# Kernel tuning notes

Measured on AMD Instinct MI355X. Metric: run time of the kernel, lower is better.

## Reference

```python
import jax, jax.numpy as jnp
import numpy as np

N_SRC = 16384
N_NBR = 16384
E = 524288
D = 128
ALPHA = 0.2  # leaky_relu slope


def setup_inputs() -> dict:
    key = jax.random.key(0)
    ks = jax.random.split(key, 16)
    s = lambda k, shape, fan: jax.random.normal(k, shape, jnp.float32) / np.sqrt(fan)
    x_cur = jax.random.normal(ks[0], (N_SRC, D), jnp.float32)
    x_nbr = jax.random.normal(ks[1], (N_NBR, D), jnp.float32)
    W1c = s(ks[2], (D, D), D); b1c = jnp.zeros((D,), jnp.float32)
    W2c = s(ks[3], (D, D), D); b2c = jnp.zeros((D,), jnp.float32)
    W1n = s(ks[4], (D, D), D); b1n = jnp.zeros((D,), jnp.float32)
    W2n = s(ks[5], (D, D), D); b2n = jnp.zeros((D,), jnp.float32)
    Wa = s(ks[6], (2 * D, 1), 2 * D); ba = jnp.zeros((1,), jnp.float32)
    src = jax.random.randint(ks[7], (E,), 0, N_SRC, jnp.int32)
    dst = jax.random.randint(ks[8], (E,), 0, N_NBR, jnp.int32)
    edges = jnp.stack([src, dst], axis=1)  # [E, 2]
    return dict(x_cur=x_cur, x_nbr=x_nbr, W1c=W1c, b1c=b1c, W2c=W2c, b2c=b2c,
                W1n=W1n, b1n=b1n, W2n=W2n, b2n=b2n, Wa=Wa, ba=ba, edges=edges)


def reference(x_cur, x_nbr, W1c, b1c, W2c, b2c, W1n, b1n, W2n, b2n, Wa, ba, edges):
    src, dst = edges[:, 0], edges[:, 1]
    # hidden MLPs (keras Dense with default activation=None -> linear stack)
    cur = (x_cur @ W1c + b1c) @ W2c + b2c          # [N_src, D]
    nbr = (x_nbr @ W1n + b1n) @ W2n + b2n          # [N_nbr, D]
    # per-edge gather + concat + attention MLP
    pair = jnp.concatenate([cur[src], nbr[dst]], axis=1)   # [E, 2D]
    scores = jax.nn.leaky_relu((pair @ Wa + ba)[:, 0], ALPHA)  # [E]
    # segment softmax over source node
    exp_s = jnp.exp(scores)
    seg_sum = jax.ops.segment_sum(exp_s, src, num_segments=N_SRC)  # [N_src]
    norm_s = exp_s / seg_sum[src]                                   # [E]
    # scatter to dense adjacency and matmul (faithful to tf.scatter_nd + matmul)
    adj = jnp.zeros((N_SRC, N_NBR), jnp.float32).at[src, dst].add(norm_s)
    return adj @ nbr                                # [N_src, D]
```

## Files before the change

kernel.cpp:

```cpp
#include <hip/hip_runtime.h>
#include <hip/hip_bf16.h>

#define NSRC 16384
#define NNBR 16384
#define NE   524288
#define DDIM 128
#define ALPHA_C 0.2f
#define CAP 128

#define GEMM_BLKS (NNBR / 32)
#define ACUR_BLKS (NSRC / 8)
#define SCAT_BLKS (NE / 512)

typedef __hip_bfloat16 bf16;

__device__ __forceinline__ float b2f(bf16 v) { return __bfloat162float(v); }
__device__ __forceinline__ float us2f(unsigned short u) {
    return __uint_as_float(((unsigned)u) << 16);
}
__device__ __forceinline__ unsigned short f2us(float f) {
    bf16 h = __float2bfloat16(f);
    return *reinterpret_cast<unsigned short*>(&h);
}
__device__ __forceinline__ float LD(const void* p, int i, bool f32) {
    return f32 ? ((const float*)p)[i] : b2f(((const bf16*)p)[i]);
}
__device__ __forceinline__ bool detect_f32(const unsigned short* xprobe, int t, int* s_flag) {
    if (t < 64) {
        int ex = (xprobe[2 * t] >> 7) & 0xFF;
        unsigned long long m = __ballot(ex >= 0xC0);
        if (t == 0) *s_flag = (__popcll(m) >= 2) ? 1 : 0;
    }
    __syncthreads();
    return *s_flag != 0;
}

__global__ __launch_bounds__(1024) void k_prep(const unsigned short* __restrict__ xprobe,
                             const void* __restrict__ W1c, const void* __restrict__ b1c,
                             const void* __restrict__ W2c, const void* __restrict__ b2c,
                             const void* __restrict__ W1n, const void* __restrict__ b1n,
                             const void* __restrict__ W2n, const void* __restrict__ b2n,
                             const void* __restrict__ Wa, const void* __restrict__ ba,
                             int* __restrict__ flagp, float* __restrict__ u_c,
                             float* __restrict__ wan, float* __restrict__ bn,
                             float* __restrict__ c0, float* __restrict__ baf,
                             float* __restrict__ M, int* __restrict__ cursor) {
    __shared__ int s_flag;
    __shared__ float tc[DDIM], wa_s[DDIM];
    __shared__ float sred[2];
    __shared__ float w1r[8][DDIM];
    int t = threadIdx.x;

    if (blockIdx.x == 17) {
#pragma unroll
        for (int i = 0; i < NSRC / 1024; i++) cursor[i * 1024 + t] = 0;
        return;
    }
    const bool f32 = detect_f32(xprobe, t, &s_flag);

    if (blockIdx.x != 0) {
        int i0 = (blockIdx.x - 1) * 8;
        int r = t >> 7, j = t & 127;
        w1r[r][j] = LD(W1n, (i0 + r) * DDIM + j, f32);
        __syncthreads();
        float s = 0.f;
        if (f32) {
            const float* p = (const float*)W2n + j;
#pragma unroll 8
            for (int k = 0; k < DDIM; k++) s += w1r[r][k] * p[k * DDIM];
        } else {
            const bf16* p = (const bf16*)W2n + j;
#pragma unroll 8
            for (int k = 0; k < DDIM; k++) s += w1r[r][k] * b2f(p[k * DDIM]);
        }
        M[(i0 + r) * DDIM + j] = s;
        return;
    }

    if (t == 0) { flagp[0] = f32 ? 1 : 0; baf[0] = LD(ba, 0, f32); }
    if (t < DDIM) wa_s[t] = LD(Wa, t, f32);
    else if (t < 2 * DDIM) wan[t - DDIM] = LD(Wa, t, f32);
    __syncthreads();

    int row = t >> 3, sub = t & 7, k0 = sub * 16;
    float s = 0.f, bb = 0.f;
    if (f32) {
        const float* w2c = (const float*)W2c + row * DDIM + k0;
        const float* b1nf = (const float*)b1n;
        const float* w2n = (const float*)W2n;
#pragma unroll
        for (int k = 0; k < 16; k++) {
            s  += w2c[k] * wa_s[k0 + k];
            bb += b1nf[k0 + k] * w2n[(k0 + k) * DDIM + row];
        }
    } else {
        const bf16* w2c = (const bf16*)W2c + row * DDIM + k0;
        const bf16* b1nh = (const bf16*)b1n;
        const bf16* w2n = (const bf16*)W2n;
#pragma unroll
        for (int k = 0; k < 16; k++) {
            s  += b2f(w2c[k]) * wa_s[k0 + k];
            bb += b2f(b1nh[k0 + k]) * b2f(w2n[(k0 + k) * DDIM + row]);
        }
    }
    s  += __shfl_xor(s, 1, 64);  s  += __shfl_xor(s, 2, 64);  s  += __shfl_xor(s, 4, 64);
    bb += __shfl_xor(bb, 1, 64); bb += __shfl_xor(bb, 2, 64); bb += __shfl_xor(bb, 4, 64);
    if (sub == 0) { tc[row] = s; bn[row] = bb + LD(b2n, row, f32); }
    __syncthreads();

    float u = 0.f;
    if (f32) {
        const float* w1c = (const float*)W1c + row * DDIM + k0;
#pragma unroll
        for (int k = 0; k < 16; k++) u += w1c[k] * tc[k0 + k];
    } else {
        const bf16* w1c = (const bf16*)W1c + row * DDIM + k0;
#pragma unroll
        for (int k = 0; k < 16; k++) u += b2f(w1c[k]) * tc[k0 + k];
    }
    u += __shfl_xor(u, 1, 64); u += __shfl_xor(u, 2, 64); u += __shfl_xor(u, 4, 64);
    if (sub == 0) u_c[row] = u;

    if (t < 128) {
        float v = LD(b1c, t, f32) * tc[t] + LD(b2c, t, f32) * wa_s[t];
#pragma unroll
        for (int o = 32; o > 0; o >>= 1) v += __shfl_down(v, o, 64);
        if ((t & 63) == 0) sred[t >> 6] = v;
    }
    __syncthreads();
    if (t == 0) c0[0] = sred[0] + sred[1];
}

__global__ __launch_bounds__(128) void k_main(const void* __restrict__ Xn,
                                              const void* __restrict__ Xc,
                                              const float* __restrict__ M,
                                              const float* __restrict__ bn,
                                              const float* __restrict__ wan,
                                              const float* __restrict__ u_c,
                                              const float* __restrict__ c0,
                                              const int* __restrict__ flagp,
                                              const int2* __restrict__ edges2,
                                              int* __restrict__ cursor,
                                              int* __restrict__ bucket,
                                              unsigned short* __restrict__ Y,
                                              float* __restrict__ a_nbr,
                                              float* __restrict__ a_cur) {
    int t = threadIdx.x;
    int b = blockIdx.x;

    if (b >= GEMM_BLKS + ACUR_BLKS) {
        int e0 = (b - GEMM_BLKS - ACUR_BLKS) * 512 + t * 4;
        int4 p0 = reinterpret_cast<const int4*>(edges2)[t + (b - GEMM_BLKS - ACUR_BLKS) * 256];
        int4 p1 = reinterpret_cast<const int4*>(edges2)[t + (b - GEMM_BLKS - ACUR_BLKS) * 256 + 128];
        (void)e0;
        int p;
        p = atomicAdd(cursor + p0.x, 1); if (p < CAP) bucket[p0.x * CAP + p] = p0.y;
        p = atomicAdd(cursor + p0.z, 1); if (p < CAP) bucket[p0.z * CAP + p] = p0.w;
        p = atomicAdd(cursor + p1.x, 1); if (p < CAP) bucket[p1.x * CAP + p] = p1.y;
        p = atomicAdd(cursor + p1.z, 1); if (p < CAP) bucket[p1.z * CAP + p] = p1.w;
        return;
    }

    bool f32 = flagp[0] != 0;
    if (b >= GEMM_BLKS) {
        int base = (b - GEMM_BLKS) * 8 + (t >> 6) * 4;
        int lane = t & 63;
        float cc = c0[0];
        float w0 = u_c[2 * lane], w1 = u_c[2 * lane + 1];
#pragma unroll
        for (int it = 0; it < 4; it++) {
            int gw = base + it;
            float v0, v1;
            if (f32) {
                float2 v = reinterpret_cast<const float2*>((const float*)Xc + (size_t)gw * DDIM)[lane];
                v0 = v.x; v1 = v.y;
            } else {
                unsigned v = reinterpret_cast<const unsigned*>((const unsigned short*)Xc + (size_t)gw * DDIM)[lane];
                v0 = us2f((unsigned short)(v & 0xffffu));
                v1 = us2f((unsigned short)(v >> 16));
            }
            float acc = v0 * w0 + v1 * w1;
#pragma unroll
            for (int o = 32; o > 0; o >>= 1) acc += __shfl_down(acc, o, 64);
            if (lane == 0) a_cur[gw] = acc + cc;
        }
        return;
    }

    __shared__ float xs[32][DDIM];
    int rg = t >> 5, cg = t & 31;
    int row0 = b * 32;
    if (f32) {
        const float4* px = reinterpret_cast<const float4*>((const float*)Xn + (size_t)row0 * DDIM);
#pragma unroll
        for (int q = 0; q < 8; q++) {
            int idx = q * 128 + t;
            float4 v = px[idx];
            int rr = idx >> 5, c = (idx & 31) * 4;
            xs[rr][c] = v.x; xs[rr][c + 1] = v.y; xs[rr][c + 2] = v.z; xs[rr][c + 3] = v.w;
        }
    } else {
        const ushort4* px = reinterpret_cast<const ushort4*>((const bf16*)Xn + (size_t)row0 * DDIM);
#pragma unroll
        for (int q = 0; q < 8; q++) {
            int idx = q * 128 + t;
            ushort4 v = px[idx];
            int rr = idx >> 5, c = (idx & 31) * 4;
            xs[rr][c] = us2f(v.x); xs[rr][c + 1] = us2f(v.y);
            xs[rr][c + 2] = us2f(v.z); xs[rr][c + 3] = us2f(v.w);
        }
    }
    __syncthreads();
    float acc[8][4];
    float4 bb = reinterpret_cast<const float4*>(bn)[cg];
#pragma unroll
    for (int rr = 0; rr < 8; rr++) {
        acc[rr][0] = bb.x; acc[rr][1] = bb.y; acc[rr][2] = bb.z; acc[rr][3] = bb.w;
    }
    const float4* Mp = reinterpret_cast<const float4*>(M) + cg;
#pragma unroll 4
    for (int k = 0; k < DDIM; k++) {
        float4 m4 = Mp[k * 32];
#pragma unroll
        for (int rr = 0; rr < 8; rr++) {
            float x = xs[rg * 8 + rr][k];
            acc[rr][0] += x * m4.x; acc[rr][1] += x * m4.y;
            acc[rr][2] += x * m4.z; acc[rr][3] += x * m4.w;
        }
    }
    float4 wn = reinterpret_cast<const float4*>(wan)[cg];
#pragma unroll
    for (int rr = 0; rr < 8; rr++) {
        int row = row0 + rg * 8 + rr;
        ushort4 y;
        y.x = f2us(acc[rr][0]); y.y = f2us(acc[rr][1]);
        y.z = f2us(acc[rr][2]); y.w = f2us(acc[rr][3]);
        reinterpret_cast<ushort4*>(Y + (size_t)row * DDIM)[cg] = y;
        float v = acc[rr][0] * wn.x + acc[rr][1] * wn.y + acc[rr][2] * wn.z + acc[rr][3] * wn.w;
        v += __shfl_xor(v, 1, 64); v += __shfl_xor(v, 2, 64); v += __shfl_xor(v, 4, 64);
        v += __shfl_xor(v, 8, 64); v += __shfl_xor(v, 16, 64);
        if (cg == 0) a_nbr[row] = v;
    }
}

__global__ __launch_bounds__(256) void k_aggregate(const int* __restrict__ cursor,
                                                   const int* __restrict__ bucket,
                                                   const float* __restrict__ a_cur,
                                                   const float* __restrict__ a_nbr,
                                                   const float* __restrict__ baf,
                                                   const unsigned short* __restrict__ nbr,
                                                   float* __restrict__ out) {
    int gw = blockIdx.x * 4 + (threadIdx.x >> 6);
    int lane = threadIdx.x & 63;
    int g = lane >> 3;
    int sub = lane & 7;
    int cnt = cursor[gw];
    cnt = cnt < CAP ? cnt : CAP;
    const int* bp = bucket + (size_t)gw * CAP;
    float acb = a_cur[gw] + baf[0];
    float acc[16];
#pragma unroll
    for (int k = 0; k < 16; k++) acc[k] = 0.f;
    float den = 0.f;

    if (cnt > 0) {
        int j = g;
        bool act = j < cnt;
        int d = act ? bp[j] : 0;
        float an = act ? a_nbr[d] : 0.f;
        uint4 v0 = make_uint4(0, 0, 0, 0), v1 = v0;
        if (act) {
            const uint4* p = reinterpret_cast<const uint4*>(nbr + (size_t)d * DDIM + sub * 16);
            v0 = p[0]; v1 = p[1];
        }
        for (int base = 0; base < cnt; base += 8) {
            int jn = base + 8 + g;
            bool actn = jn < cnt;
            int dn = 0; float ann = 0.f;
            uint4 n0 = make_uint4(0, 0, 0, 0), n1 = n0;
            if (actn) {
                dn = bp[jn];
                ann = a_nbr[dn];
                const uint4* p = reinterpret_cast<const uint4*>(nbr + (size_t)dn * DDIM + sub * 16);
                n0 = p[0]; n1 = p[1];
            }
            float sc = acb + an;
            sc = sc > 0.f ? sc : ALPHA_C * sc;
            sc = fminf(sc, 80.f);
            float w = act ? __expf(sc) : 0.f;
            den += w;
            acc[0]  += w * us2f((unsigned short)(v0.x & 0xffffu));
            acc[1]  += w * us2f((unsigned short)(v0.x >> 16));
            acc[2]  += w * us2f((unsigned short)(v0.y & 0xffffu));
            acc[3]  += w * us2f((unsigned short)(v0.y >> 16));
            acc[4]  += w * us2f((unsigned short)(v0.z & 0xffffu));
            acc[5]  += w * us2f((unsigned short)(v0.z >> 16));
            acc[6]  += w * us2f((unsigned short)(v0.w & 0xffffu));
            acc[7]  += w * us2f((unsigned short)(v0.w >> 16));
            acc[8]  += w * us2f((unsigned short)(v1.x & 0xffffu));
            acc[9]  += w * us2f((unsigned short)(v1.x >> 16));
            acc[10] += w * us2f((unsigned short)(v1.y & 0xffffu));
            acc[11] += w * us2f((unsigned short)(v1.y >> 16));
            acc[12] += w * us2f((unsigned short)(v1.z & 0xffffu));
            acc[13] += w * us2f((unsigned short)(v1.z >> 16));
            acc[14] += w * us2f((unsigned short)(v1.w & 0xffffu));
            acc[15] += w * us2f((unsigned short)(v1.w >> 16));
            an = ann; v0 = n0; v1 = n1; act = actn;
        }
    }
#pragma unroll
    for (int k = 0; k < 16; k++) {
        acc[k] += __shfl_xor(acc[k], 8, 64);
        acc[k] += __shfl_xor(acc[k], 16, 64);
        acc[k] += __shfl_xor(acc[k], 32, 64);
    }
    den += __shfl_xor(den, 8, 64);
    den += __shfl_xor(den, 16, 64);
    den += __shfl_xor(den, 32, 64);
    float inv = den > 0.f ? 1.f / den : 0.f;
    if (g == 0) {
        float4* po = reinterpret_cast<float4*>(out + (size_t)gw * DDIM + sub * 16);
        po[0] = make_float4(acc[0] * inv, acc[1] * inv, acc[2] * inv, acc[3] * inv);
        po[1] = make_float4(acc[4] * inv, acc[5] * inv, acc[6] * inv, acc[7] * inv);
        po[2] = make_float4(acc[8] * inv, acc[9] * inv, acc[10] * inv, acc[11] * inv);
        po[3] = make_float4(acc[12] * inv, acc[13] * inv, acc[14] * inv, acc[15] * inv);
    }
}

extern "C" void kernel_launch(void* const* d_in, const int* in_sizes, int n_in,
                              void* d_out, int out_size, void* d_ws, size_t ws_size,
                              hipStream_t stream) {
    const void* x_cur = d_in[0];
    const void* x_nbr = d_in[1];
    const void* W1c = d_in[2];
    const void* b1c = d_in[3];
    const void* W2c = d_in[4];
    const void* b2c = d_in[5];
    const void* W1n = d_in[6];
    const void* b1n = d_in[7];
    const void* W2n = d_in[8];
    const void* b2n = d_in[9];
    const void* Wa  = d_in[10];
    const void* ba  = d_in[11];
    const int2* edges2 = (const int2*)d_in[12];
    float* out = (float*)d_out;

    char* w = (char*)d_ws;
    size_t off = 0;
    auto alloc = [&](size_t b) { size_t o = off; off = (off + b + 255) & ~(size_t)255; return o; };
    float* M      = (float*)(w + alloc(DDIM * DDIM * 4));
    float* u_c    = (float*)(w + alloc(DDIM * 4));
    float* wan    = (float*)(w + alloc(DDIM * 4));
    float* bn     = (float*)(w + alloc(DDIM * 4));
    float* c0     = (float*)(w + alloc(4));
    float* baf    = (float*)(w + alloc(4));
    int*   flag   = (int*)(w + alloc(4));
    float* a_cur  = (float*)(w + alloc(NSRC * 4));
    float* a_nbr  = (float*)(w + alloc(NNBR * 4));
    int* cursor   = (int*)(w + alloc(NSRC * 4));
    int* bucket   = (int*)(w + alloc((size_t)NSRC * CAP * 4));
    unsigned short* nbr = (unsigned short*)(w + alloc((size_t)NNBR * DDIM * 2));

    k_prep<<<18, 1024, 0, stream>>>((const unsigned short*)x_cur, W1c, b1c, W2c, b2c,
                                    W1n, b1n, W2n, b2n, Wa, ba, flag, u_c, wan, bn, c0, baf,
                                    M, cursor);
    k_main<<<GEMM_BLKS + ACUR_BLKS + SCAT_BLKS, 128, 0, stream>>>(
        x_nbr, x_cur, M, bn, wan, u_c, c0, flag, edges2, cursor, bucket, nbr, a_nbr, a_cur);
    k_aggregate<<<NSRC / 4, 256, 0, stream>>>(cursor, bucket, a_cur, a_nbr, baf, nbr, out);
}
```

Before: 157.5 us.

## Reorder block roles, bf16 smem GEMM tile, nontemporal bucket stores, deeper gather prefetch

The fused main kernel now puts the edge-bucketing blocks first so the atomic-heavy scatter work starts earliest, and the bucket writes use nontemporal stores. The neighbor GEMM keeps its input tile in shared memory as bf16 rather than f32, halving LDS footprint, and processes four k-steps per iteration with vector loads. The aggregation loop double-buffers two edge groups in flight instead of one, raising memory-level parallelism for the gathers. Rounding f32 inputs to bf16 in the GEMM changes precision when inputs are f32; masked lanes now rely on exp(-1e30) underflowing to zero.

```diff
diff --git a/kernel.cpp b/kernel.cpp
--- a/kernel.cpp
+++ b/kernel.cpp
@@ -8,9 +8,9 @@
 #define ALPHA_C 0.2f
 #define CAP 128
 
+#define SCAT_BLKS (NE / 512)
 #define GEMM_BLKS (NNBR / 32)
 #define ACUR_BLKS (NSRC / 8)
-#define SCAT_BLKS (NE / 512)
 
 typedef __hip_bfloat16 bf16;
 
@@ -148,22 +148,24 @@
     int t = threadIdx.x;
     int b = blockIdx.x;
 
-    if (b >= GEMM_BLKS + ACUR_BLKS) {
-        int e0 = (b - GEMM_BLKS - ACUR_BLKS) * 512 + t * 4;
-        int4 p0 = reinterpret_cast<const int4*>(edges2)[t + (b - GEMM_BLKS - ACUR_BLKS) * 256];
-        int4 p1 = reinterpret_cast<const int4*>(edges2)[t + (b - GEMM_BLKS - ACUR_BLKS) * 256 + 128];
-        (void)e0;
+    if (b < SCAT_BLKS) {
+        int4 p0 = reinterpret_cast<const int4*>(edges2)[t + b * 256];
+        int4 p1 = reinterpret_cast<const int4*>(edges2)[t + b * 256 + 128];
         int p;
-        p = atomicAdd(cursor + p0.x, 1); if (p < CAP) bucket[p0.x * CAP + p] = p0.y;
-        p = atomicAdd(cursor + p0.z, 1); if (p < CAP) bucket[p0.z * CAP + p] = p0.w;
-        p = atomicAdd(cursor + p1.x, 1); if (p < CAP) bucket[p1.x * CAP + p] = p1.y;
-        p = atomicAdd(cursor + p1.z, 1); if (p < CAP) bucket[p1.z * CAP + p] = p1.w;
+        p = atomicAdd(cursor + p0.x, 1);
+        if (p < CAP) __builtin_nontemporal_store(p0.y, &bucket[p0.x * CAP + p]);
+        p = atomicAdd(cursor + p0.z, 1);
+        if (p < CAP) __builtin_nontemporal_store(p0.w, &bucket[p0.z * CAP + p]);
+        p = atomicAdd(cursor + p1.x, 1);
+        if (p < CAP) __builtin_nontemporal_store(p1.y, &bucket[p1.x * CAP + p]);
+        p = atomicAdd(cursor + p1.z, 1);
+        if (p < CAP) __builtin_nontemporal_store(p1.w, &bucket[p1.z * CAP + p]);
         return;
     }
 
     bool f32 = flagp[0] != 0;
-    if (b >= GEMM_BLKS) {
-        int base = (b - GEMM_BLKS) * 8 + (t >> 6) * 4;
+    if (b >= SCAT_BLKS + GEMM_BLKS) {
+        int base = (b - SCAT_BLKS - GEMM_BLKS) * 8 + (t >> 6) * 4;
         int lane = t & 63;
         float cc = c0[0];
         float w0 = u_c[2 * lane], w1 = u_c[2 * lane + 1];
@@ -187,9 +189,9 @@
         return;
     }
 
-    __shared__ float xs[32][DDIM];
+    __shared__ unsigned short xs[32][DDIM];
     int rg = t >> 5, cg = t & 31;
-    int row0 = b * 32;
+    int row0 = (b - SCAT_BLKS) * 32;
     if (f32) {
         const float4* px = reinterpret_cast<const float4*>((const float*)Xn + (size_t)row0 * DDIM);
 #pragma unroll
@@ -197,17 +199,16 @@
             int idx = q * 128 + t;
             float4 v = px[idx];
             int rr = idx >> 5, c = (idx & 31) * 4;
-            xs[rr][c] = v.x; xs[rr][c + 1] = v.y; xs[rr][c + 2] = v.z; xs[rr][c + 3] = v.w;
+            ushort4 y; y.x = f2us(v.x); y.y = f2us(v.y); y.z = f2us(v.z); y.w = f2us(v.w);
+            *reinterpret_cast<ushort4*>(&xs[rr][c]) = y;
         }
     } else {
         const ushort4* px = reinterpret_cast<const ushort4*>((const bf16*)Xn + (size_t)row0 * DDIM);
 #pragma unroll
         for (int q = 0; q < 8; q++) {
             int idx = q * 128 + t;
-            ushort4 v = px[idx];
             int rr = idx >> 5, c = (idx & 31) * 4;
-            xs[rr][c] = us2f(v.x); xs[rr][c + 1] = us2f(v.y);
-            xs[rr][c + 2] = us2f(v.z); xs[rr][c + 3] = us2f(v.w);
+            *reinterpret_cast<ushort4*>(&xs[rr][c]) = px[idx];
         }
     }
     __syncthreads();
@@ -218,14 +219,20 @@
         acc[rr][0] = bb.x; acc[rr][1] = bb.y; acc[rr][2] = bb.z; acc[rr][3] = bb.w;
     }
     const float4* Mp = reinterpret_cast<const float4*>(M) + cg;
-#pragma unroll 4
-    for (int k = 0; k < DDIM; k++) {
-        float4 m4 = Mp[k * 32];
+#pragma unroll 2
+    for (int k0 = 0; k0 < DDIM; k0 += 4) {
+        float4 m0 = Mp[(k0 + 0) * 32];
+        float4 m1 = Mp[(k0 + 1) * 32];
+        float4 m2 = Mp[(k0 + 2) * 32];
+        float4 m3 = Mp[(k0 + 3) * 32];
 #pragma unroll
         for (int rr = 0; rr < 8; rr++) {
-            float x = xs[rg * 8 + rr][k];
-            acc[rr][0] += x * m4.x; acc[rr][1] += x * m4.y;
-            acc[rr][2] += x * m4.z; acc[rr][3] += x * m4.w;
+            ushort4 xk = *reinterpret_cast<const ushort4*>(&xs[rg * 8 + rr][k0]);
+            float x0 = us2f(xk.x), x1 = us2f(xk.y), x2 = us2f(xk.z), x3 = us2f(xk.w);
+            acc[rr][0] += x0 * m0.x + x1 * m1.x + x2 * m2.x + x3 * m3.x;
+            acc[rr][1] += x0 * m0.y + x1 * m1.y + x2 * m2.y + x3 * m3.y;
+            acc[rr][2] += x0 * m0.z + x1 * m1.z + x2 * m2.z + x3 * m3.z;
+            acc[rr][3] += x0 * m0.w + x1 * m1.w + x2 * m2.w + x3 * m3.w;
         }
     }
     float4 wn = reinterpret_cast<const float4*>(wan)[cg];
@@ -258,56 +265,63 @@
     cnt = cnt < CAP ? cnt : CAP;
     const int* bp = bucket + (size_t)gw * CAP;
     float acb = a_cur[gw] + baf[0];
+    const uint4 z4 = make_uint4(0, 0, 0, 0);
     float acc[16];
 #pragma unroll
     for (int k = 0; k < 16; k++) acc[k] = 0.f;
     float den = 0.f;
 
+#define LOADE(J, Dv, ANv, V0v, V1v)                                                  \
+    do {                                                                             \
+        int j_ = (J); bool a_ = j_ < cnt;                                            \
+        Dv = a_ ? bp[j_] : 0;                                                        \
+        ANv = a_ ? a_nbr[Dv] : -1e30f;                                               \
+        if (a_) {                                                                    \
+            const uint4* p_ = reinterpret_cast<const uint4*>(nbr + (size_t)Dv * DDIM + sub * 16); \
+            V0v = p_[0]; V1v = p_[1];                                                \
+        } else { V0v = z4; V1v = z4; }                                               \
+    } while (0)
+
+#define CONSUME(ANv, V0v, V1v)                                                       \
+    do {                                                                             \
+        float sc_ = acb + ANv;                                                       \
+        sc_ = sc_ > 0.f ? sc_ : ALPHA_C * sc_;                                       \
+        sc_ = fminf(sc_, 80.f);                                                      \
+        float w_ = __expf(sc_);                                                      \
+        den += w_;                                                                   \
+        acc[0]  += w_ * us2f((unsigned short)(V0v.x & 0xffffu));                     \
+        acc[1]  += w_ * us2f((unsigned short)(V0v.x >> 16));                         \
+        acc[2]  += w_ * us2f((unsigned short)(V0v.y & 0xffffu));                     \
+        acc[3]  += w_ * us2f((unsigned short)(V0v.y >> 16));                         \
+        acc[4]  += w_ * us2f((unsigned short)(V0v.z & 0xffffu));                     \
+        acc[5]  += w_ * us2f((unsigned short)(V0v.z >> 16));                         \
+        acc[6]  += w_ * us2f((unsigned short)(V0v.w & 0xffffu));                     \
+        acc[7]  += w_ * us2f((unsigned short)(V0v.w >> 16));                         \
+        acc[8]  += w_ * us2f((unsigned short)(V1v.x & 0xffffu));                     \
+        acc[9]  += w_ * us2f((unsigned short)(V1v.x >> 16));                         \
+        acc[10] += w_ * us2f((unsigned short)(V1v.y & 0xffffu));                     \
+        acc[11] += w_ * us2f((unsigned short)(V1v.y >> 16));                         \
+        acc[12] += w_ * us2f((unsigned short)(V1v.z & 0xffffu));                     \
+        acc[13] += w_ * us2f((unsigned short)(V1v.z >> 16));                         \
+        acc[14] += w_ * us2f((unsigned short)(V1v.w & 0xffffu));                     \
+        acc[15] += w_ * us2f((unsigned short)(V1v.w >> 16));                         \
+    } while (0)
+
     if (cnt > 0) {
-        int j = g;
-        bool act = j < cnt;
-        int d = act ? bp[j] : 0;
-        float an = act ? a_nbr[d] : 0.f;
-        uint4 v0 = make_uint4(0, 0, 0, 0), v1 = v0;
-        if (act) {
-            const uint4* p = reinterpret_cast<const uint4*>(nbr + (size_t)d * DDIM + sub * 16);
-            v0 = p[0]; v1 = p[1];
-        }
-        for (int base = 0; base < cnt; base += 8) {
-            int jn = base + 8 + g;
-            bool actn = jn < cnt;
-            int dn = 0; float ann = 0.f;
-            uint4 n0 = make_uint4(0, 0, 0, 0), n1 = n0;
-            if (actn) {
-                dn = bp[jn];
-                ann = a_nbr[dn];
-                const uint4* p = reinterpret_cast<const uint4*>(nbr + (size_t)dn * DDIM + sub * 16);
-                n0 = p[0]; n1 = p[1];
-            }
-            float sc = acb + an;
-            sc = sc > 0.f ? sc : ALPHA_C * sc;
-            sc = fminf(sc, 80.f);
-            float w = act ? __expf(sc) : 0.f;
-            den += w;
-            acc[0]  += w * us2f((unsigned short)(v0.x & 0xffffu));
-            acc[1]  += w * us2f((unsigned short)(v0.x >> 16));
-            acc[2]  += w * us2f((unsigned short)(v0.y & 0xffffu));
-            acc[3]  += w * us2f((unsigned short)(v0.y >> 16));
-            acc[4]  += w * us2f((unsigned short)(v0.z & 0xffffu));
-            acc[5]  += w * us2f((unsigned short)(v0.z >> 16));
-            acc[6]  += w * us2f((unsigned short)(v0.w & 0xffffu));
-            acc[7]  += w * us2f((unsigned short)(v0.w >> 16));
-            acc[8]  += w * us2f((unsigned short)(v1.x & 0xffffu));
-            acc[9]  += w * us2f((unsigned short)(v1.x >> 16));
-            acc[10] += w * us2f((unsigned short)(v1.y & 0xffffu));
-            acc[11] += w * us2f((unsigned short)(v1.y >> 16));
-            acc[12] += w * us2f((unsigned short)(v1.z & 0xffffu));
-            acc[13] += w * us2f((unsigned short)(v1.z >> 16));
-            acc[14] += w * us2f((unsigned short)(v1.w & 0xffffu));
-            acc[15] += w * us2f((unsigned short)(v1.w >> 16));
-            an = ann; v0 = n0; v1 = n1; act = actn;
-        }
-    }
+        int dA; float anA; uint4 vA0, vA1;
+        int dB; float anB; uint4 vB0, vB1;
+        LOADE(g, dA, anA, vA0, vA1);
+        LOADE(8 + g, dB, anB, vB0, vB1);
+        for (int base = 0; base < cnt; base += 16) {
+            CONSUME(anA, vA0, vA1);
+            LOADE(base + 16 + g, dA, anA, vA0, vA1);
+            CONSUME(anB, vB0, vB1);
+            LOADE(base + 24 + g, dB, anB, vB0, vB1);
+        }
+    }
+#undef LOADE
+#undef CONSUME
+
 #pragma unroll
     for (int k = 0; k < 16; k++) {
         acc[k] += __shfl_xor(acc[k], 8, 64);
@@ -364,7 +378,7 @@
     k_prep<<<18, 1024, 0, stream>>>((const unsigned short*)x_cur, W1c, b1c, W2c, b2c,
                                     W1n, b1n, W2n, b2n, Wa, ba, flag, u_c, wan, bn, c0, baf,
                                     M, cursor);
-    k_main<<<GEMM_BLKS + ACUR_BLKS + SCAT_BLKS, 128, 0, stream>>>(
+    k_main<<<SCAT_BLKS + GEMM_BLKS + ACUR_BLKS, 128, 0, stream>>>(
         x_nbr, x_cur, M, bn, wan, u_c, c0, flag, edges2, cursor, bucket, nbr, a_nbr, a_cur);
     k_aggregate<<<NSRC / 4, 256, 0, stream>>>(cursor, bucket, a_cur, a_nbr, baf, nbr, out);
 }
```

Result: slower. 166.6 us (+5.8%).
